# Kernel optimization log

Measured on AMD Instinct MI355X. Metric: run time of the kernel, lower is better.

The kernel has to match this reference:

```python
import jax, jax.numpy as jnp
import numpy as np

EMBED_DIM = 2048
NUM_HEADS = 16
HEAD_DIM = EMBED_DIM // NUM_HEADS
B, T = 4, 2048


def setup_inputs() -> dict:
    key = jax.random.key(0)
    ks = jax.random.split(key, 9)
    s = 1.0 / np.sqrt(EMBED_DIM)
    x = jax.random.normal(ks[0], (B, T, EMBED_DIM), dtype=jnp.float32)
    Wq = jax.random.normal(ks[1], (EMBED_DIM, EMBED_DIM), dtype=jnp.float32) * s
    bq = jnp.zeros((EMBED_DIM,), dtype=jnp.float32)
    Wk = jax.random.normal(ks[2], (EMBED_DIM, EMBED_DIM), dtype=jnp.float32) * s
    bk = jnp.zeros((EMBED_DIM,), dtype=jnp.float32)
    Wv = jax.random.normal(ks[3], (EMBED_DIM, EMBED_DIM), dtype=jnp.float32) * s
    bv = jnp.zeros((EMBED_DIM,), dtype=jnp.float32)
    Wo = jax.random.normal(ks[4], (EMBED_DIM, EMBED_DIM), dtype=jnp.float32) * s
    bo = jnp.zeros((EMBED_DIM,), dtype=jnp.float32)
    return {"x": x, "Wq": Wq, "bq": bq, "Wk": Wk, "bk": bk,
            "Wv": Wv, "bv": bv, "Wo": Wo, "bo": bo}


def reference(x, Wq, bq, Wk, bk, Wv, bv, Wo, bo):
    Bb, Tt, C = x.shape
    H, D = NUM_HEADS, C // NUM_HEADS
    # QKV projections (Linear: x @ W.T + b), reshape to [B, H, T, D]
    q = (jnp.einsum('btc,oc->bto', x, Wq) + bq).reshape(Bb, Tt, H, D).transpose(0, 2, 1, 3)
    k = (jnp.einsum('btc,oc->bto', x, Wk) + bk).reshape(Bb, Tt, H, D).transpose(0, 2, 1, 3)
    v = (jnp.einsum('btc,oc->bto', x, Wv) + bv).reshape(Bb, Tt, H, D).transpose(0, 2, 1, 3)
    logits = jnp.einsum('bhqd,bhkd->bhqk', q, k) / jnp.sqrt(jnp.float32(D))
    causal = jnp.triu(jnp.ones((Tt, Tt), dtype=bool), 1)  # True above diagonal
    logits = jnp.where(causal, -jnp.inf, logits)
    attn = jax.nn.softmax(logits, axis=-1)
    out = jnp.einsum('bhqk,bhkd->bhqd', attn, v)  # [B, H, T, D]
    out = out.transpose(0, 2, 1, 3).reshape(Bb, Tt, C)
    y = jnp.einsum('btc,oc->bto', out, Wo) + bo
    return y
```

## Files before the change

### kernel.cpp

```cpp
#include <hip/hip_runtime.h>
#include <hip/hip_bf16.h>
#include <cstdint>
#include <cstddef>

typedef __attribute__((ext_vector_type(8))) short short8;
typedef __attribute__((ext_vector_type(4))) short short4_;
typedef __attribute__((ext_vector_type(4))) float floatx4;
typedef __attribute__((ext_vector_type(4))) unsigned short ushort4_;

#define MFMA16(a, b, c) __builtin_amdgcn_mfma_f32_16x16x32_bf16((a), (b), (c), 0, 0, 0)

__device__ __forceinline__ unsigned short f2bf(float f) {
  __hip_bfloat16 h = __float2bfloat16(f);
  return *reinterpret_cast<unsigned short*>(&h);
}

__device__ __forceinline__ void gl_lds16(const void* g, void* lds) {
  __builtin_amdgcn_global_load_lds(
      (const __attribute__((address_space(1))) void*)g,
      (__attribute__((address_space(3))) void*)lds, 16, 0, 0);
}

__global__ void cast_f32_bf16(const float* __restrict__ in, __hip_bfloat16* __restrict__ out) {
  const int i = (blockIdx.x * 256 + threadIdx.x) * 4;
  const float4 v = *reinterpret_cast<const float4*>(in + i);
  ushort4_ o = { f2bf(v.x), f2bf(v.y), f2bf(v.z), f2bf(v.w) };
  *reinterpret_cast<ushort4_*>(out + i) = o;
}

template <int MODE>
__global__ __launch_bounds__(512, 2)
void gemm256(const __hip_bfloat16* __restrict__ Ap, const __hip_bfloat16* __restrict__ Bp,
             const float* __restrict__ bias, void* __restrict__ Cout,
             int M, int N, int K) {
  __shared__ __align__(16) __hip_bfloat16 SA[4][256 * 32];
  __shared__ __align__(16) __hip_bfloat16 SB[4][256 * 32];

  const int tid = threadIdx.x;
  const int wid = tid >> 6, lane = tid & 63;
  const int wr = wid >> 2, wc = wid & 3;
  const int g = lane >> 4, c16 = lane & 15;

  const int swzb = (blockIdx.x & 7) * 32 + (blockIdx.x >> 3);
  const int bm = swzb >> 3, bn = swzb & 7;

  const int srow = lane >> 2;
  const int slog = (lane & 3) ^ ((lane >> 3) & 3);
  const int swz = c16 * 32 + (g ^ ((c16 >> 1) & 3)) * 8;

  floatx4 acc[8][4] = {};

  auto stage = [&](int kt) {
    const int kb = kt * 32;
    const int slot = kt & 3;
#pragma unroll
    for (int i = 0; i < 2; ++i) {
      const int rbase = i * 128 + wid * 16;
      gl_lds16(Ap + (size_t)(bm * 256 + rbase + srow) * K + kb + slog * 8,
               SA[slot] + rbase * 32);
      gl_lds16(Bp + (size_t)(bn * 256 + rbase + srow) * K + kb + slog * 8,
               SB[slot] + rbase * 32);
    }
  };

  auto compute = [&](int slot) {
    const __hip_bfloat16* sa = SA[slot];
    const __hip_bfloat16* sb = SB[slot];
    short8 af[8], bf[4];
#pragma unroll
    for (int m = 0; m < 8; ++m)
      af[m] = *reinterpret_cast<const short8*>(sa + wr * 4096 + m * 512 + swz);
#pragma unroll
    for (int n = 0; n < 4; ++n)
      bf[n] = *reinterpret_cast<const short8*>(sb + wc * 2048 + n * 512 + swz);
    __builtin_amdgcn_s_setprio(1);
#pragma unroll
    for (int m = 0; m < 8; ++m)
#pragma unroll
      for (int n = 0; n < 4; ++n)
        acc[m][n] = MFMA16(af[m], bf[n], acc[m][n]);
    __builtin_amdgcn_s_setprio(0);
  };

  const int nkt = K >> 5;
  stage(0); stage(1); stage(2);

  for (int kt = 0; kt < nkt - 3; ++kt) {
    asm volatile("s_waitcnt vmcnt(8)" ::: "memory");
    __builtin_amdgcn_s_barrier();
    stage(kt + 3);
    compute(kt & 3);
  }
  asm volatile("s_waitcnt vmcnt(8)" ::: "memory");
  __builtin_amdgcn_s_barrier();
  compute((nkt - 3) & 3);
  asm volatile("s_waitcnt vmcnt(4)" ::: "memory");
  __builtin_amdgcn_s_barrier();
  compute((nkt - 2) & 3);
  asm volatile("s_waitcnt vmcnt(0)" ::: "memory");
  __builtin_amdgcn_s_barrier();
  compute((nkt - 1) & 3);

#pragma unroll
  for (int n = 0; n < 4; ++n) {
    const int colg = bn * 256 + wc * 64 + n * 16 + c16;
    const float bv = bias[colg];
#pragma unroll
    for (int m = 0; m < 8; ++m) {
      const int rowg = bm * 256 + wr * 128 + m * 16 + g * 4;
      if (MODE == 0) {
        __hip_bfloat16* C = (__hip_bfloat16*)Cout;
#pragma unroll
        for (int j = 0; j < 4; ++j)
          C[(size_t)(rowg + j) * N + colg] = __float2bfloat16(acc[m][n][j] + bv);
      } else if (MODE == 1) {
        __hip_bfloat16* C = (__hip_bfloat16*)Cout;
        const int bb = rowg >> 11, t0 = rowg & 2047;
        ushort4_ pk = { f2bf(acc[m][n][0] + bv), f2bf(acc[m][n][1] + bv),
                        f2bf(acc[m][n][2] + bv), f2bf(acc[m][n][3] + bv) };
        *reinterpret_cast<ushort4_*>(C + ((size_t)bb * 2048 + colg) * 2048 + t0) = pk;
      } else {
        float* C = (float*)Cout;
#pragma unroll
        for (int j = 0; j < 4; ++j)
          C[(size_t)(rowg + j) * N + colg] = acc[m][n][j] + bv;
      }
    }
  }
}

__global__ __launch_bounds__(256, 2)
void attn_fwd4(const __hip_bfloat16* __restrict__ Q, const __hip_bfloat16* __restrict__ K,
               const __hip_bfloat16* __restrict__ Vt, __hip_bfloat16* __restrict__ ctx) {
  constexpr int T = 2048, C = 2048, D = 128;
  __shared__ __align__(16) __hip_bfloat16 Ks[64][136];
  __shared__ __align__(16) __hip_bfloat16 Vs[128][64];
  __shared__ __align__(16) __hip_bfloat16 Pl[4][32][64];

  const int tid = threadIdx.x;
  const int w = tid >> 6, lane = tid & 63;
  const int g = lane >> 4, c16 = lane & 15;

  const int bid = blockIdx.x;
  const int swz = (bid & 7) * 128 + (bid >> 3);
  const int bh = swz >> 4, qb = 15 - (swz & 15);
  const int b = bh >> 4, h = bh & 15;
  const int wq = qb * 128 + w * 32;

  const __hip_bfloat16* Qh = Q + (size_t)b * T * C + h * D;
  const __hip_bfloat16* Kh = K + (size_t)b * T * C + h * D;
  const __hip_bfloat16* Vh = Vt + (size_t)bh * D * T;

  short8 qf[2][4];
#pragma unroll
  for (int m = 0; m < 2; ++m)
#pragma unroll
    for (int kk = 0; kk < 4; ++kk)
      qf[m][kk] = *reinterpret_cast<const short8*>(Qh + (size_t)(wq + m * 16 + c16) * C + kk * 32 + g * 8);

  floatx4 acc[2][8] = {};
  float mrow[2] = {-INFINITY, -INFINITY};
  float lrow[2] = {0.f, 0.f};

  const float scale = 0.08838834764831845f;
  const int krow = tid >> 4, kcol = (tid & 15) * 8;
  const int vrow = tid >> 3;
  const int vslot = (tid & 7) ^ (vrow & 7);
  const int vgcol = (tid & 7) * 8;

  short8 kr[4], vr[4];
  auto gloadK = [&](int kb) {
#pragma unroll
    for (int p = 0; p < 4; ++p)
      kr[p] = *reinterpret_cast<const short8*>(Kh + (size_t)(kb + p * 16 + krow) * C + kcol);
  };
  auto gloadV = [&](int kb) {
#pragma unroll
    for (int p = 0; p < 4; ++p)
      vr[p] = *reinterpret_cast<const short8*>(Vh + (size_t)(p * 32 + vrow) * T + kb + vgcol);
  };

  __hip_bfloat16 (*Pq)[64] = Pl[w];
  const int nkt = qb * 2 + 2;
  gloadK(0);
  gloadV(0);

  for (int kt = 0; kt < nkt; ++kt) {
    const int kb = kt * 64;
    __syncthreads();
#pragma unroll
    for (int p = 0; p < 4; ++p)
      *reinterpret_cast<short8*>(&Ks[p * 16 + krow][kcol]) = kr[p];
#pragma unroll
    for (int p = 0; p < 4; ++p)
      *reinterpret_cast<short8*>(&Vs[p * 32 + vrow][vslot * 8]) = vr[p];
    __syncthreads();

    const bool hasnext = (kt + 1 < nkt);
    const bool part = (kb <= wq + 31);
    if (hasnext) gloadK(kb + 64);

    if (part) {
      const bool needmask = (kb + 63 > wq);
      floatx4 s[2][4] = {};
      __builtin_amdgcn_s_setprio(1);
#pragma unroll
      for (int n = 0; n < 4; ++n)
#pragma unroll
        for (int kk = 0; kk < 4; ++kk) {
          short8 kf = *reinterpret_cast<const short8*>(&Ks[n * 16 + c16][kk * 32 + g * 8]);
          s[0][n] = MFMA16(kf, qf[0][kk], s[0][n]);
          s[1][n] = MFMA16(kf, qf[1][kk], s[1][n]);
        }
      __builtin_amdgcn_s_setprio(0);
      float vmax[2];
#pragma unroll
      for (int m = 0; m < 2; ++m) {
        const int q = wq + m * 16 + c16;
        float vm = -INFINITY;
#pragma unroll
        for (int n = 0; n < 4; ++n)
#pragma unroll
          for (int j = 0; j < 4; ++j) {
            float a = s[m][n][j] * scale;
            if (needmask && (kb + n * 16 + g * 4 + j > q)) a = -INFINITY;
            s[m][n][j] = a;
            vm = fmaxf(vm, a);
          }
        vm = fmaxf(vm, __shfl_xor(vm, 16));
        vm = fmaxf(vm, __shfl_xor(vm, 32));
        vmax[m] = vm;
      }
      const float grow = fmaxf(vmax[0] - mrow[0], vmax[1] - mrow[1]);
      const bool nore = __all(grow <= 8.0f);
#pragma unroll
      for (int m = 0; m < 2; ++m) {
        const float mn = nore ? mrow[m] : fmaxf(mrow[m], vmax[m]);
        float rs = 0.f;
#pragma unroll
        for (int n = 0; n < 4; ++n) {
          float p0 = __expf(s[m][n][0] - mn), p1 = __expf(s[m][n][1] - mn);
          float p2 = __expf(s[m][n][2] - mn), p3 = __expf(s[m][n][3] - mn);
          rs += (p0 + p1) + (p2 + p3);
          ushort4_ pk = { f2bf(p0), f2bf(p1), f2bf(p2), f2bf(p3) };
          *reinterpret_cast<ushort4_*>(&Pq[m * 16 + c16][((4 * n + g) ^ c16) * 4]) = pk;
        }
        rs += __shfl_xor(rs, 16);
        rs += __shfl_xor(rs, 32);
        if (nore) {
          lrow[m] += rs;
        } else {
          const float sc = __expf(mrow[m] - mn);
          lrow[m] = lrow[m] * sc + rs;
          mrow[m] = mn;
#pragma unroll
          for (int dt = 0; dt < 8; ++dt)
#pragma unroll
            for (int j = 0; j < 4; ++j) acc[m][dt][j] *= sc;
        }
      }
    }
    if (hasnext) gloadV(kb + 64);
    if (part) {
      short8 pb[2][2];
#pragma unroll
      for (int m = 0; m < 2; ++m)
#pragma unroll
        for (int ks = 0; ks < 2; ++ks) {
          short4_ lo = *reinterpret_cast<const short4_*>(&Pq[m * 16 + c16][((8 * ks + 2 * g) ^ c16) * 4]);
          short4_ hi = *reinterpret_cast<const short4_*>(&Pq[m * 16 + c16][((8 * ks + 2 * g + 1) ^ c16) * 4]);
          short8 r;
          r[0] = lo[0]; r[1] = lo[1]; r[2] = lo[2]; r[3] = lo[3];
          r[4] = hi[0]; r[5] = hi[1]; r[6] = hi[2]; r[7] = hi[3];
          pb[m][ks] = r;
        }
      __builtin_amdgcn_s_setprio(1);
#pragma unroll
      for (int dt = 0; dt < 8; ++dt)
#pragma unroll
        for (int ks = 0; ks < 2; ++ks) {
          const int pslot = ((ks * 4 + g) ^ (c16 & 7)) * 8;
          short8 vf = *reinterpret_cast<const short8*>(&Vs[dt * 16 + c16][pslot]);
          acc[0][dt] = MFMA16(vf, pb[0][ks], acc[0][dt]);
          acc[1][dt] = MFMA16(vf, pb[1][ks], acc[1][dt]);
        }
      __builtin_amdgcn_s_setprio(0);
    }
  }

#pragma unroll
  for (int m = 0; m < 2; ++m) {
    const float inv = 1.0f / lrow[m];
    const size_t row = (size_t)b * T + wq + m * 16 + c16;
#pragma unroll
    for (int dt = 0; dt < 8; ++dt) {
      ushort4_ o = { f2bf(acc[m][dt][0] * inv), f2bf(acc[m][dt][1] * inv),
                     f2bf(acc[m][dt][2] * inv), f2bf(acc[m][dt][3] * inv) };
      *reinterpret_cast<ushort4_*>(ctx + row * C + h * D + dt * 16 + g * 4) = o;
    }
  }
}

extern "C" void kernel_launch(void* const* d_in, const int* in_sizes, int n_in,
                              void* d_out, int out_size, void* d_ws, size_t ws_size,
                              hipStream_t stream) {
  const float* x  = (const float*)d_in[0];
  const float* Wq = (const float*)d_in[1];
  const float* bq = (const float*)d_in[2];
  const float* Wk = (const float*)d_in[3];
  const float* bk = (const float*)d_in[4];
  const float* Wv = (const float*)d_in[5];
  const float* bv = (const float*)d_in[6];
  const float* Wo = (const float*)d_in[7];
  const float* bo = (const float*)d_in[8];

  const int M = 8192, N = 2048, K = 2048;
  const size_t MB = 1u << 20;
  char* ws = (char*)d_ws;
  __hip_bfloat16* xb  = (__hip_bfloat16*)(ws);
  __hip_bfloat16* wqb = (__hip_bfloat16*)(ws + 32 * MB);
  __hip_bfloat16* wkb = (__hip_bfloat16*)(ws + 40 * MB);
  __hip_bfloat16* wvb = (__hip_bfloat16*)(ws + 48 * MB);
  __hip_bfloat16* wob = (__hip_bfloat16*)(ws + 56 * MB);
  __hip_bfloat16* Qb  = (__hip_bfloat16*)(ws + 64 * MB);
  __hip_bfloat16* Kb  = (__hip_bfloat16*)(ws + 96 * MB);
  __hip_bfloat16* Vtb = (__hip_bfloat16*)(ws + 128 * MB);
  if (ws_size < 160 * MB) return;

  cast_f32_bf16<<<(M * N) / 1024, 256, 0, stream>>>(x, xb);
  cast_f32_bf16<<<(N * K) / 1024, 256, 0, stream>>>(Wq, wqb);
  cast_f32_bf16<<<(N * K) / 1024, 256, 0, stream>>>(Wk, wkb);
  cast_f32_bf16<<<(N * K) / 1024, 256, 0, stream>>>(Wv, wvb);
  cast_f32_bf16<<<(N * K) / 1024, 256, 0, stream>>>(Wo, wob);

  const dim3 gg((M / 256) * (N / 256));
  gemm256<0><<<gg, 512, 0, stream>>>(xb, wqb, bq, Qb, M, N, K);
  gemm256<0><<<gg, 512, 0, stream>>>(xb, wkb, bk, Kb, M, N, K);
  gemm256<1><<<gg, 512, 0, stream>>>(xb, wvb, bv, Vtb, M, N, K);

  attn_fwd4<<<64 * 16, 256, 0, stream>>>(Qb, Kb, Vtb, xb);

  gemm256<2><<<gg, 512, 0, stream>>>(xb, wob, bo, d_out, M, N, K);
}
```

Measured before the change: 534.2 us.

## Fuse QKV projections into one GEMM, merge casts, use exp2 softmax

Merges the five f32→bf16 cast launches into one kernel and runs the Q, K and V projections as a single GEMM with N=6144 against concatenated weights. The epilogue sends each column segment to the Q, K or transposed-V buffer. The attention softmax now folds log2(e) into the scale and uses exp2f instead of __expf. The aim is fewer launches and one larger, better-filled GEMM grid with less per-kernel tail overhead, at the cost of a more complex epilogue and a changed block swizzle mapping.

```diff
diff --git a/kernel.cpp b/kernel.cpp
--- a/kernel.cpp
+++ b/kernel.cpp
@@ -21,17 +21,32 @@
       (__attribute__((address_space(3))) void*)lds, 16, 0, 0);
 }
 
-__global__ void cast_f32_bf16(const float* __restrict__ in, __hip_bfloat16* __restrict__ out) {
-  const int i = (blockIdx.x * 256 + threadIdx.x) * 4;
-  const float4 v = *reinterpret_cast<const float4*>(in + i);
+__global__ void cast5_f32_bf16(const float* __restrict__ x, const float* __restrict__ wq,
+                               const float* __restrict__ wk, const float* __restrict__ wv,
+                               const float* __restrict__ wo,
+                               __hip_bfloat16* __restrict__ xb, __hip_bfloat16* __restrict__ wqb,
+                               __hip_bfloat16* __restrict__ wkb, __hip_bfloat16* __restrict__ wvb,
+                               __hip_bfloat16* __restrict__ wob) {
+  const int bid = blockIdx.x;
+  const float* src;
+  __hip_bfloat16* dst;
+  int base;
+  if (bid < 16384)      { src = x;  dst = xb;  base = bid; }
+  else if (bid < 20480) { src = wq; dst = wqb; base = bid - 16384; }
+  else if (bid < 24576) { src = wk; dst = wkb; base = bid - 20480; }
+  else if (bid < 28672) { src = wv; dst = wvb; base = bid - 24576; }
+  else                  { src = wo; dst = wob; base = bid - 28672; }
+  const int i = base * 1024 + threadIdx.x * 4;
+  const float4 v = *reinterpret_cast<const float4*>(src + i);
   ushort4_ o = { f2bf(v.x), f2bf(v.y), f2bf(v.z), f2bf(v.w) };
-  *reinterpret_cast<ushort4_*>(out + i) = o;
+  *reinterpret_cast<ushort4_*>(dst + i) = o;
 }
 
 template <int MODE>
 __global__ __launch_bounds__(512, 2)
 void gemm256(const __hip_bfloat16* __restrict__ Ap, const __hip_bfloat16* __restrict__ Bp,
-             const float* __restrict__ bias, void* __restrict__ Cout,
+             const float* __restrict__ b0, const float* __restrict__ b1,
+             const float* __restrict__ b2, void* __restrict__ Cout,
              int M, int N, int K) {
   __shared__ __align__(16) __hip_bfloat16 SA[4][256 * 32];
   __shared__ __align__(16) __hip_bfloat16 SB[4][256 * 32];
@@ -41,8 +56,10 @@
   const int wr = wid >> 2, wc = wid & 3;
   const int g = lane >> 4, c16 = lane & 15;
 
-  const int swzb = (blockIdx.x & 7) * 32 + (blockIdx.x >> 3);
-  const int bm = swzb >> 3, bn = swzb & 7;
+  const int nbn = N >> 8;
+  const int cpx = gridDim.x >> 3;
+  const int swzb = (blockIdx.x & 7) * cpx + (blockIdx.x >> 3);
+  const int bm = swzb / nbn, bn = swzb % nbn;
 
   const int srow = lane >> 2;
   const int slog = (lane & 3) ^ ((lane >> 3) & 3);
@@ -104,21 +121,31 @@
 #pragma unroll
   for (int n = 0; n < 4; ++n) {
     const int colg = bn * 256 + wc * 64 + n * 16 + c16;
-    const float bv = bias[colg];
+    int seg = 0, colh = colg;
+    float bv;
+    if (MODE == 3) {
+      seg = colg >> 11;
+      colh = colg & 2047;
+      bv = (seg == 0 ? b0 : (seg == 1 ? b1 : b2))[colh];
+    } else {
+      bv = b0[colg];
+    }
 #pragma unroll
     for (int m = 0; m < 8; ++m) {
       const int rowg = bm * 256 + wr * 128 + m * 16 + g * 4;
-      if (MODE == 0) {
-        __hip_bfloat16* C = (__hip_bfloat16*)Cout;
-#pragma unroll
-        for (int j = 0; j < 4; ++j)
-          C[(size_t)(rowg + j) * N + colg] = __float2bfloat16(acc[m][n][j] + bv);
-      } else if (MODE == 1) {
-        __hip_bfloat16* C = (__hip_bfloat16*)Cout;
-        const int bb = rowg >> 11, t0 = rowg & 2047;
-        ushort4_ pk = { f2bf(acc[m][n][0] + bv), f2bf(acc[m][n][1] + bv),
-                        f2bf(acc[m][n][2] + bv), f2bf(acc[m][n][3] + bv) };
-        *reinterpret_cast<ushort4_*>(C + ((size_t)bb * 2048 + colg) * 2048 + t0) = pk;
+      if (MODE == 3) {
+        if (seg < 2) {
+          __hip_bfloat16* C = (__hip_bfloat16*)Cout + (size_t)seg * 16777216u;
+#pragma unroll
+          for (int j = 0; j < 4; ++j)
+            C[(size_t)(rowg + j) * 2048 + colh] = __float2bfloat16(acc[m][n][j] + bv);
+        } else {
+          __hip_bfloat16* C = (__hip_bfloat16*)Cout + (size_t)2 * 16777216u;
+          const int bb = rowg >> 11, t0 = rowg & 2047;
+          ushort4_ pk = { f2bf(acc[m][n][0] + bv), f2bf(acc[m][n][1] + bv),
+                          f2bf(acc[m][n][2] + bv), f2bf(acc[m][n][3] + bv) };
+          *reinterpret_cast<ushort4_*>(C + ((size_t)bb * 2048 + colh) * 2048 + t0) = pk;
+        }
       } else {
         float* C = (float*)Cout;
 #pragma unroll
@@ -162,7 +189,7 @@
   float mrow[2] = {-INFINITY, -INFINITY};
   float lrow[2] = {0.f, 0.f};
 
-  const float scale = 0.08838834764831845f;
+  const float scale2 = 0.12751744f;
   const int krow = tid >> 4, kcol = (tid & 15) * 8;
   const int vrow = tid >> 3;
   const int vslot = (tid & 7) ^ (vrow & 7);
@@ -222,7 +249,7 @@
         for (int n = 0; n < 4; ++n)
 #pragma unroll
           for (int j = 0; j < 4; ++j) {
-            float a = s[m][n][j] * scale;
+            float a = s[m][n][j] * scale2;
             if (needmask && (kb + n * 16 + g * 4 + j > q)) a = -INFINITY;
             s[m][n][j] = a;
             vm = fmaxf(vm, a);
@@ -239,8 +266,8 @@
         float rs = 0.f;
 #pragma unroll
         for (int n = 0; n < 4; ++n) {
-          float p0 = __expf(s[m][n][0] - mn), p1 = __expf(s[m][n][1] - mn);
-          float p2 = __expf(s[m][n][2] - mn), p3 = __expf(s[m][n][3] - mn);
+          float p0 = exp2f(s[m][n][0] - mn), p1 = exp2f(s[m][n][1] - mn);
+          float p2 = exp2f(s[m][n][2] - mn), p3 = exp2f(s[m][n][3] - mn);
           rs += (p0 + p1) + (p2 + p3);
           ushort4_ pk = { f2bf(p0), f2bf(p1), f2bf(p2), f2bf(p3) };
           *reinterpret_cast<ushort4_*>(&Pq[m * 16 + c16][((4 * n + g) ^ c16) * 4]) = pk;
@@ -250,7 +277,7 @@
         if (nore) {
           lrow[m] += rs;
         } else {
-          const float sc = __expf(mrow[m] - mn);
+          const float sc = exp2f(mrow[m] - mn);
           lrow[m] = lrow[m] * sc + rs;
           mrow[m] = mn;
 #pragma unroll
@@ -314,31 +341,26 @@
   const float* Wo = (const float*)d_in[7];
   const float* bo = (const float*)d_in[8];
 
-  const int M = 8192, N = 2048, K = 2048;
+  const int M = 8192, K = 2048;
   const size_t MB = 1u << 20;
   char* ws = (char*)d_ws;
-  __hip_bfloat16* xb  = (__hip_bfloat16*)(ws);
-  __hip_bfloat16* wqb = (__hip_bfloat16*)(ws + 32 * MB);
-  __hip_bfloat16* wkb = (__hip_bfloat16*)(ws + 40 * MB);
-  __hip_bfloat16* wvb = (__hip_bfloat16*)(ws + 48 * MB);
-  __hip_bfloat16* wob = (__hip_bfloat16*)(ws + 56 * MB);
-  __hip_bfloat16* Qb  = (__hip_bfloat16*)(ws + 64 * MB);
-  __hip_bfloat16* Kb  = (__hip_bfloat16*)(ws + 96 * MB);
-  __hip_bfloat16* Vtb = (__hip_bfloat16*)(ws + 128 * MB);
+  __hip_bfloat16* xb   = (__hip_bfloat16*)(ws);
+  __hip_bfloat16* wqkv = (__hip_bfloat16*)(ws + 32 * MB);
+  __hip_bfloat16* wkb  = (__hip_bfloat16*)(ws + 40 * MB);
+  __hip_bfloat16* wvb  = (__hip_bfloat16*)(ws + 48 * MB);
+  __hip_bfloat16* wob  = (__hip_bfloat16*)(ws + 56 * MB);
+  __hip_bfloat16* Qb   = (__hip_bfloat16*)(ws + 64 * MB);
+  __hip_bfloat16* Kb   = (__hip_bfloat16*)(ws + 96 * MB);
+  __hip_bfloat16* Vtb  = (__hip_bfloat16*)(ws + 128 * MB);
   if (ws_size < 160 * MB) return;
 
-  cast_f32_bf16<<<(M * N) / 1024, 256, 0, stream>>>(x, xb);
-  cast_f32_bf16<<<(N * K) / 1024, 256, 0, stream>>>(Wq, wqb);
-  cast_f32_bf16<<<(N * K) / 1024, 256, 0, stream>>>(Wk, wkb);
-  cast_f32_bf16<<<(N * K) / 1024, 256, 0, stream>>>(Wv, wvb);
-  cast_f32_bf16<<<(N * K) / 1024, 256, 0, stream>>>(Wo, wob);
-
-  const dim3 gg((M / 256) * (N / 256));
-  gemm256<0><<<gg, 512, 0, stream>>>(xb, wqb, bq, Qb, M, N, K);
-  gemm256<0><<<gg, 512, 0, stream>>>(xb, wkb, bk, Kb, M, N, K);
-  gemm256<1><<<gg, 512, 0, stream>>>(xb, wvb, bv, Vtb, M, N, K);
+  cast5_f32_bf16<<<32768, 256, 0, stream>>>(x, Wq, Wk, Wv, Wo, xb, wqkv, wkb, wvb, wob);
+
+  gemm256<3><<<dim3((M / 256) * (6144 / 256)), 512, 0, stream>>>(
+      xb, wqkv, bq, bk, bv, Qb, M, 6144, K);
 
   attn_fwd4<<<64 * 16, 256, 0, stream>>>(Qb, Kb, Vtb, xb);
 
-  gemm256<2><<<gg, 512, 0, stream>>>(xb, wob, bo, d_out, M, N, K);
-}
+  gemm256<2><<<dim3((M / 256) * (2048 / 256)), 512, 0, stream>>>(
+      xb, wob, bo, bo, bo, d_out, M, 2048, K);
+}
```

New measurement: 548.1 us. 2.6% more time.
